# Optimization experiments

Hardware: AMD Instinct MI355X
Metric: run time of the kernel (lower is better)

The kernel has to match this reference:

```python
import jax, jax.numpy as jnp
import numpy as np

DIM = 512
HEADS = 8
WIN = 64
HIDDEN = 2048
EPS = 1e-5


def layernorm(x, g, b):
    mu = jnp.mean(x, axis=-1, keepdims=True)
    var = jnp.var(x, axis=-1, keepdims=True)
    return (x - mu) * jax.lax.rsqrt(var + EPS) * g + b


def setup_inputs() -> dict:
    key = jax.random.key(0)
    ks = jax.random.split(key, 10)
    s = lambda fan_in: 1.0 / np.sqrt(fan_in)
    return {
        "x": jax.random.normal(ks[0], (8, 4096, DIM), dtype=jnp.float32),
        "ln1_g": jnp.ones((DIM,), jnp.float32),
        "ln1_b": jnp.zeros((DIM,), jnp.float32),
        "qkv_w": jax.random.normal(ks[1], (DIM, 3 * DIM), jnp.float32) * s(DIM),
        "qkv_b": jnp.zeros((3 * DIM,), jnp.float32),
        "proj_w": jax.random.normal(ks[2], (DIM, DIM), jnp.float32) * s(DIM),
        "proj_b": jnp.zeros((DIM,), jnp.float32),
        "ln2_g": jnp.ones((DIM,), jnp.float32),
        "ln2_b": jnp.zeros((DIM,), jnp.float32),
        "fc1_w": jax.random.normal(ks[3], (DIM, HIDDEN), jnp.float32) * s(DIM),
        "fc1_b": jnp.zeros((HIDDEN,), jnp.float32),
        "fc2_w": jax.random.normal(ks[4], (HIDDEN, DIM), jnp.float32) * s(HIDDEN),
        "fc2_b": jnp.zeros((DIM,), jnp.float32),
    }


def reference(x, ln1_g, ln1_b, qkv_w, qkv_b, proj_w, proj_b, ln2_g, ln2_b,
              fc1_w, fc1_b, fc2_w, fc2_b):
    B, N, C = x.shape
    hd = C // HEADS
    scale = hd ** -0.5

    # --- W-MSA (shift_size forced to 0, attn_mask None) ---
    h = layernorm(x, ln1_g, ln1_b)
    hw = h.reshape(B * (N // WIN), WIN, C)
    qkv = hw @ qkv_w + qkv_b
    qkv = qkv.reshape(-1, WIN, 3, HEADS, hd)
    q = qkv[:, :, 0] * scale
    k = qkv[:, :, 1]
    v = qkv[:, :, 2]
    attn = jnp.einsum('bqhd,bkhd->bhqk', q, k)
    attn = jax.nn.softmax(attn, axis=-1)
    o = jnp.einsum('bhqk,bkhd->bqhd', attn, v).reshape(-1, WIN, C)
    o = o @ proj_w + proj_b
    x = x + o.reshape(B, N, C)

    # --- MLP (GELU exact, dropout=0) ---
    h2 = layernorm(x, ln2_g, ln2_b)
    h2 = jax.nn.gelu(h2 @ fc1_w + fc1_b, approximate=False)
    x = x + (h2 @ fc2_w + fc2_b)
    return x
```

## Files before the change

kernel.cpp:

```cpp
#include <hip/hip_runtime.h>
#include <hip/hip_bf16.h>
#include <cstdint>

typedef unsigned short U16;
typedef float f32x4 __attribute__((ext_vector_type(4)));
typedef __bf16 bf16x8 __attribute__((ext_vector_type(8)));

#define DEVINL __device__ __forceinline__

DEVINL U16 f2bf(float f) {
    unsigned u = __float_as_uint(f);
    return (U16)((u + 0x7FFFu + ((u >> 16) & 1u)) >> 16);
}
DEVINL float bf2f(U16 s) { return __uint_as_float(((unsigned)s) << 16); }

DEVINL void gld16(const void* g, void* l) {
    __builtin_amdgcn_global_load_lds(
        (const __attribute__((address_space(1))) void*)g,
        (__attribute__((address_space(3))) void*)l, 16, 0, 0);
}

#define MFMA_BF16 __builtin_amdgcn_mfma_f32_16x16x32_bf16

__global__ __launch_bounds__(256) void tcast_kernel(const float* __restrict__ w,
                                                    U16* __restrict__ wt, int K, int N) {
    __shared__ float tile[32][33];
    int n0 = blockIdx.x * 32, k0 = blockIdx.y * 32;
    int tx = threadIdx.x, ty = threadIdx.y;
#pragma unroll
    for (int i = 0; i < 32; i += 8) tile[ty + i][tx] = w[(size_t)(k0 + ty + i) * N + (n0 + tx)];
    __syncthreads();
#pragma unroll
    for (int i = 0; i < 32; i += 8) wt[(size_t)(n0 + ty + i) * K + (k0 + tx)] = f2bf(tile[tx][ty + i]);
}

__global__ __launch_bounds__(256) void ln_kernel(const float* __restrict__ x,
                                                 const float* __restrict__ g,
                                                 const float* __restrict__ b,
                                                 U16* __restrict__ out) {
    int lane = threadIdx.x & 63;
    size_t row = (size_t)blockIdx.x * 4 + (threadIdx.x >> 6);
    const float4* xr = (const float4*)(x + row * 512);
    float4 v0 = xr[lane], v1 = xr[lane + 64];
    float s = (v0.x + v0.y) + (v0.z + v0.w) + (v1.x + v1.y) + (v1.z + v1.w);
    float sq = (v0.x * v0.x + v0.y * v0.y + v0.z * v0.z + v0.w * v0.w) +
               (v1.x * v1.x + v1.y * v1.y + v1.z * v1.z + v1.w * v1.w);
#pragma unroll
    for (int m = 1; m < 64; m <<= 1) { s += __shfl_xor(s, m); sq += __shfl_xor(sq, m); }
    float mu = s * (1.f / 512.f);
    float var = sq * (1.f / 512.f) - mu * mu;
    float rs = rsqrtf(var + 1e-5f);
    const float4* g4 = (const float4*)g;
    const float4* b4 = (const float4*)b;
    float4 gv = g4[lane], bv = b4[lane];
    ushort4 o;
    o.x = f2bf((v0.x - mu) * rs * gv.x + bv.x);
    o.y = f2bf((v0.y - mu) * rs * gv.y + bv.y);
    o.z = f2bf((v0.z - mu) * rs * gv.z + bv.z);
    o.w = f2bf((v0.w - mu) * rs * gv.w + bv.w);
    ((ushort4*)(out + row * 512))[lane] = o;
    gv = g4[lane + 64]; bv = b4[lane + 64];
    o.x = f2bf((v1.x - mu) * rs * gv.x + bv.x);
    o.y = f2bf((v1.y - mu) * rs * gv.y + bv.y);
    o.z = f2bf((v1.z - mu) * rs * gv.z + bv.z);
    o.w = f2bf((v1.w - mu) * rs * gv.w + bv.w);
    ((ushort4*)(out + row * 512))[lane + 64] = o;
}

template <int EPI, int K>
__global__ __launch_bounds__(256, 4) void gemm_rt(const U16* __restrict__ A,
                                                  const U16* __restrict__ Bt,
                                                  const float* __restrict__ bias,
                                                  const float* __restrict__ resid,
                                                  U16* __restrict__ outb,
                                                  float* __restrict__ outf,
                                                  int M, int N, int gridN) {
    __shared__ __align__(16) U16 smem[24576];

    const int tid = threadIdx.x;
    const int lane = tid & 63, wv = tid >> 6;
    const int lo = lane & 15, hi = lane >> 4;
    const int wm = wv >> 1, wn = wv & 1;

    const int nwg = gridDim.x, bid = blockIdx.x;
    const int swzb = (bid & 7) * (nwg >> 3) + (bid >> 3);
    const int bn = swzb % gridN, bm = swzb / gridN;

    const int sr = tid >> 2;
    const int lc = (tid & 3) ^ ((sr >> 1) & 3);
    const U16* gA0 = A + (size_t)(bm * 128 + sr) * K + lc * 8;
    const U16* gA1 = gA0 + (size_t)64 * K;
    const U16* gB0 = Bt + (size_t)(bn * 128 + sr) * K + lc * 8;
    const U16* gB1 = gB0 + (size_t)64 * K;

#define STAGE(t2)                                                     \
    do {                                                              \
        U16* _l = smem + ((t2) % 3) * 8192 + tid * 8;                 \
        gld16(gA0 + (t2) * 32, _l);                                   \
        gld16(gA1 + (t2) * 32, _l + 2048);                            \
        gld16(gB0 + (t2) * 32, _l + 4096);                            \
        gld16(gB1 + (t2) * 32, _l + 6144);                            \
    } while (0)

    const int ck = (hi ^ ((lo >> 1) & 3)) << 3;
    const int aoff = (wm * 64 + lo) * 32 + ck;
    const int boff = 4096 + (wn * 64 + lo) * 32 + ck;

    f32x4 acc[4][4] = {};

    constexpr int NT = K >> 5;
    static_assert(NT >= 16 && (NT % 16) == 0, "K must be a multiple of 512");

    STAGE(0);
    STAGE(1);

#define ITER(t)                                                                 \
    do {                                                                        \
        if ((t) + 1 < NT) {                                                     \
            asm volatile("s_waitcnt vmcnt(4)" ::: "memory");                    \
        } else {                                                                \
            asm volatile("s_waitcnt vmcnt(0)" ::: "memory");                    \
        }                                                                       \
        __builtin_amdgcn_s_barrier();                                           \
        if ((t) + 2 < NT) STAGE((t) + 2);                                       \
        {                                                                       \
            const int _cb = ((t) % 3) * 8192;                                   \
            const U16* _Ab = smem + _cb + aoff;                                 \
            const U16* _Bb = smem + _cb + boff;                                 \
            bf16x8 af[4], bg[4];                                                \
            _Pragma("unroll") for (int i = 0; i < 4; ++i)                       \
                af[i] = *(const bf16x8*)(_Ab + i * 512);                        \
            _Pragma("unroll") for (int j = 0; j < 4; ++j)                       \
                bg[j] = *(const bf16x8*)(_Bb + j * 512);                        \
            __builtin_amdgcn_s_setprio(1);                                      \
            _Pragma("unroll") for (int i = 0; i < 4; ++i)                       \
                _Pragma("unroll") for (int j = 0; j < 4; ++j)                   \
                    acc[i][j] = MFMA_BF16(af[i], bg[j], acc[i][j], 0, 0, 0);    \
            __builtin_amdgcn_s_setprio(0);                                      \
        }                                                                       \
    } while (0)

#pragma unroll
    for (int t0 = 0; t0 < NT; t0 += 16) {
#pragma unroll
        for (int tt = 0; tt < 16; ++tt) ITER(t0 + tt);
    }

    const int row0 = bm * 128 + wm * 64 + hi * 4;
    const int col0 = bn * 128 + wn * 64 + lo;
    float bc[4];
#pragma unroll
    for (int j = 0; j < 4; ++j) bc[j] = bias[col0 + j * 16];

    if (EPI == 1) {
#pragma unroll
        for (int i = 0; i < 4; ++i)
#pragma unroll
            for (int r = 0; r < 4; ++r) {
                const size_t rowb = (size_t)(row0 + i * 16 + r) * N;
#pragma unroll
                for (int j = 0; j < 4; ++j) {
                    const size_t idx = rowb + col0 + j * 16;
                    outf[idx] = acc[i][j][r] + bc[j] + resid[idx];
                }
            }
    } else {
#pragma unroll
        for (int i = 0; i < 4; ++i)
#pragma unroll
            for (int j = 0; j < 4; ++j)
#pragma unroll
                for (int r = 0; r < 4; ++r) {
                    float v = acc[i][j][r] + bc[j];
                    if (EPI == 2) {
                        float u = v * (0.7978845608028654f + 0.0356774081f * v * v);
                        v = v / (1.f + __expf(-2.f * u));
                    }
                    outb[(size_t)(row0 + i * 16 + r) * N + col0 + j * 16] = f2bf(v);
                }
    }
#undef ITER
#undef STAGE
}

__global__ __launch_bounds__(256) void attn_kernel(const U16* __restrict__ qkv,
                                                   U16* __restrict__ o) {
    const int blk = blockIdx.x;
    const int w = blk >> 3, h = blk & 7;
    const int tid = threadIdx.x;
    const int lane = tid & 63, wv = tid >> 6;
    const int lo = lane & 15, hi = lane >> 4;

    __shared__ __align__(16) U16 Qs[64][72];
    __shared__ __align__(16) U16 Ks[64][72];
    __shared__ __align__(16) U16 Vt[64][72];
    __shared__ __align__(16) U16 Ps[4][16][72];

    {
        const int r = tid >> 2;
        const int c0 = (tid & 3) << 4;
        const U16* p = qkv + (size_t)(w * 64 + r) * 1536 + h * 64 + c0;
        *(bf16x8*)&Ks[r][c0] = *(const bf16x8*)(p + 512);
        *(bf16x8*)&Ks[r][c0 + 8] = *(const bf16x8*)(p + 520);
        const U16* pv = p + 1024;
#pragma unroll
        for (int i = 0; i < 16; i++) Vt[c0 + i][r] = pv[i];
#pragma unroll
        for (int i = 0; i < 16; i++) Qs[r][c0 + i] = f2bf(bf2f(p[i]) * 0.125f);
    }
    __syncthreads();

    const int rb = wv * 16;
    f32x4 s[4] = {};
#pragma unroll
    for (int dc = 0; dc < 64; dc += 32) {
        bf16x8 a = *(const bf16x8*)&Qs[rb + lo][dc + hi * 8];
#pragma unroll
        for (int jb = 0; jb < 4; jb++) {
            bf16x8 bfr = *(const bf16x8*)&Ks[jb * 16 + lo][dc + hi * 8];
            s[jb] = MFMA_BF16(a, bfr, s[jb], 0, 0, 0);
        }
    }
#pragma unroll
    for (int r = 0; r < 4; r++) {
        float m = fmaxf(fmaxf(s[0][r], s[1][r]), fmaxf(s[2][r], s[3][r]));
#pragma unroll
        for (int msk = 1; msk < 16; msk <<= 1) m = fmaxf(m, __shfl_xor(m, msk));
        float e[4], sum = 0.f;
#pragma unroll
        for (int jb = 0; jb < 4; jb++) { e[jb] = __expf(s[jb][r] - m); sum += e[jb]; }
#pragma unroll
        for (int msk = 1; msk < 16; msk <<= 1) sum += __shfl_xor(sum, msk);
        float inv = 1.f / sum;
#pragma unroll
        for (int jb = 0; jb < 4; jb++) Ps[wv][hi * 4 + r][jb * 16 + lo] = f2bf(e[jb] * inv);
    }
    __syncthreads();

    f32x4 oa[4] = {};
#pragma unroll
    for (int jc = 0; jc < 64; jc += 32) {
        bf16x8 a = *(const bf16x8*)&Ps[wv][lo][jc + hi * 8];
#pragma unroll
        for (int db = 0; db < 4; db++) {
            bf16x8 bfr = *(const bf16x8*)&Vt[db * 16 + lo][jc + hi * 8];
            oa[db] = MFMA_BF16(a, bfr, oa[db], 0, 0, 0);
        }
    }
#pragma unroll
    for (int db = 0; db < 4; db++)
#pragma unroll
        for (int r = 0; r < 4; r++)
            o[(size_t)(w * 64 + rb + hi * 4 + r) * 512 + h * 64 + db * 16 + lo] = f2bf(oa[db][r]);
}

extern "C" void kernel_launch(void* const* d_in, const int* in_sizes, int n_in,
                              void* d_out, int out_size, void* d_ws, size_t ws_size,
                              hipStream_t stream) {
    const float* x = (const float*)d_in[0];
    const float* ln1_g = (const float*)d_in[1];
    const float* ln1_b = (const float*)d_in[2];
    const float* qkv_w = (const float*)d_in[3];
    const float* qkv_b = (const float*)d_in[4];
    const float* proj_w = (const float*)d_in[5];
    const float* proj_b = (const float*)d_in[6];
    const float* ln2_g = (const float*)d_in[7];
    const float* ln2_b = (const float*)d_in[8];
    const float* fc1_w = (const float*)d_in[9];
    const float* fc1_b = (const float*)d_in[10];
    const float* fc2_w = (const float*)d_in[11];
    const float* fc2_b = (const float*)d_in[12];
    float* out = (float*)d_out;

    char* ws = (char*)d_ws;
    U16* hbuf = (U16*)ws;
    U16* big = (U16*)(ws + 33554432);
    U16* wt_qkv = (U16*)(ws + 33554432 + 134217728);
    U16* wt_proj = wt_qkv + 1536 * 512;
    U16* wt_fc1 = wt_proj + 512 * 512;
    U16* wt_fc2 = wt_fc1 + 2048 * 512;

    dim3 tb(32, 8);
    tcast_kernel<<<dim3(1536 / 32, 512 / 32), tb, 0, stream>>>(qkv_w, wt_qkv, 512, 1536);
    tcast_kernel<<<dim3(512 / 32, 512 / 32), tb, 0, stream>>>(proj_w, wt_proj, 512, 512);
    tcast_kernel<<<dim3(2048 / 32, 512 / 32), tb, 0, stream>>>(fc1_w, wt_fc1, 512, 2048);
    tcast_kernel<<<dim3(512 / 32, 2048 / 32), tb, 0, stream>>>(fc2_w, wt_fc2, 2048, 512);

    ln_kernel<<<8192, 256, 0, stream>>>(x, ln1_g, ln1_b, hbuf);
    gemm_rt<0, 512><<<3072, 256, 0, stream>>>(hbuf, wt_qkv, qkv_b, nullptr, big, nullptr, 32768, 1536, 12);
    attn_kernel<<<4096, 256, 0, stream>>>(big, hbuf);
    gemm_rt<1, 512><<<1024, 256, 0, stream>>>(hbuf, wt_proj, proj_b, x, nullptr, out, 32768, 512, 4);
    ln_kernel<<<8192, 256, 0, stream>>>(out, ln2_g, ln2_b, hbuf);
    gemm_rt<2, 512><<<4096, 256, 0, stream>>>(hbuf, wt_fc1, fc1_b, nullptr, big, nullptr, 32768, 2048, 16);
    gemm_rt<1, 2048><<<1024, 256, 0, stream>>>(big, wt_fc2, fc2_b, out, nullptr, out, 32768, 512, 4);
}
```

Before: 380.5 us.

## Enlarge GEMM tiles to 256x256 with 8 waves and a four-stage LDS ring

The GEMM block tile grows from 128x128 to 256x256, using 512 threads. Each wave now computes a 128x64 sub-tile, and the LDS ring grows to four stages (128KB). A and B tile loads are issued as separate prefetches interleaved between two MFMA half-phases. The goal is more operand reuse per byte loaded and better overlap of global-to-LDS traffic with compute. In exchange, each CU holds only one block, the accumulator register load is larger, and the proj and fc2 GEMMs launch only 256 blocks, which risks tail and latency-hiding problems.

```diff
diff --git a/kernel.cpp b/kernel.cpp
--- a/kernel.cpp
+++ b/kernel.cpp
@@ -68,19 +68,19 @@
 }
 
 template <int EPI, int K>
-__global__ __launch_bounds__(256, 4) void gemm_rt(const U16* __restrict__ A,
+__global__ __launch_bounds__(512, 1) void gemm_rt(const U16* __restrict__ A,
                                                   const U16* __restrict__ Bt,
                                                   const float* __restrict__ bias,
                                                   const float* __restrict__ resid,
                                                   U16* __restrict__ outb,
                                                   float* __restrict__ outf,
                                                   int M, int N, int gridN) {
-    __shared__ __align__(16) U16 smem[24576];
+    __shared__ __align__(16) U16 smem[65536];
 
     const int tid = threadIdx.x;
     const int lane = tid & 63, wv = tid >> 6;
     const int lo = lane & 15, hi = lane >> 4;
-    const int wm = wv >> 1, wn = wv & 1;
+    const int wm = wv >> 2, wn = wv & 3;
 
     const int nwg = gridDim.x, bid = blockIdx.x;
     const int swzb = (bid & 7) * (nwg >> 3) + (bid >> 3);
@@ -88,31 +88,35 @@
 
     const int sr = tid >> 2;
     const int lc = (tid & 3) ^ ((sr >> 1) & 3);
-    const U16* gA0 = A + (size_t)(bm * 128 + sr) * K + lc * 8;
-    const U16* gA1 = gA0 + (size_t)64 * K;
-    const U16* gB0 = Bt + (size_t)(bn * 128 + sr) * K + lc * 8;
-    const U16* gB1 = gB0 + (size_t)64 * K;
-
-#define STAGE(t2)                                                     \
+    const U16* gA0 = A + (size_t)(bm * 256 + sr) * K + lc * 8;
+    const U16* gA1 = gA0 + (size_t)128 * K;
+    const U16* gB0 = Bt + (size_t)(bn * 256 + sr) * K + lc * 8;
+    const U16* gB1 = gB0 + (size_t)128 * K;
+
+#define STAGE_A(t2)                                                   \
     do {                                                              \
-        U16* _l = smem + ((t2) % 3) * 8192 + tid * 8;                 \
+        U16* _l = smem + ((t2) & 3) * 16384 + tid * 8;                \
         gld16(gA0 + (t2) * 32, _l);                                   \
-        gld16(gA1 + (t2) * 32, _l + 2048);                            \
-        gld16(gB0 + (t2) * 32, _l + 4096);                            \
-        gld16(gB1 + (t2) * 32, _l + 6144);                            \
+        gld16(gA1 + (t2) * 32, _l + 4096);                            \
     } while (0)
+#define STAGE_B(t2)                                                   \
+    do {                                                              \
+        U16* _l = smem + ((t2) & 3) * 16384 + 8192 + tid * 8;         \
+        gld16(gB0 + (t2) * 32, _l);                                   \
+        gld16(gB1 + (t2) * 32, _l + 4096);                            \
+    } while (0)
 
     const int ck = (hi ^ ((lo >> 1) & 3)) << 3;
-    const int aoff = (wm * 64 + lo) * 32 + ck;
-    const int boff = 4096 + (wn * 64 + lo) * 32 + ck;
-
-    f32x4 acc[4][4] = {};
+    const int aoff = (wm * 128 + lo) * 32 + ck;
+    const int boff = 8192 + (wn * 64 + lo) * 32 + ck;
+
+    f32x4 acc[8][4] = {};
 
     constexpr int NT = K >> 5;
     static_assert(NT >= 16 && (NT % 16) == 0, "K must be a multiple of 512");
 
-    STAGE(0);
-    STAGE(1);
+    STAGE_A(0); STAGE_B(0);
+    STAGE_A(1); STAGE_B(1);
 
 #define ITER(t)                                                                 \
     do {                                                                        \
@@ -122,11 +126,12 @@
             asm volatile("s_waitcnt vmcnt(0)" ::: "memory");                    \
         }                                                                       \
         __builtin_amdgcn_s_barrier();                                           \
-        if ((t) + 2 < NT) STAGE((t) + 2);                                       \
         {                                                                       \
-            const int _cb = ((t) % 3) * 8192;                                   \
+            const int _cb = ((t) & 3) * 16384;                                  \
             const U16* _Ab = smem + _cb + aoff;                                 \
             const U16* _Bb = smem + _cb + boff;                                 \
+               \
+            if ((t) + 2 < NT) STAGE_A((t) + 2);                                 \
             bf16x8 af[4], bg[4];                                                \
             _Pragma("unroll") for (int i = 0; i < 4; ++i)                       \
                 af[i] = *(const bf16x8*)(_Ab + i * 512);                        \
@@ -137,6 +142,16 @@
                 _Pragma("unroll") for (int j = 0; j < 4; ++j)                   \
                     acc[i][j] = MFMA_BF16(af[i], bg[j], acc[i][j], 0, 0, 0);    \
             __builtin_amdgcn_s_setprio(0);                                      \
+                              \
+            if ((t) + 2 < NT) STAGE_B((t) + 2);                                 \
+            bf16x8 af2[4];                                                      \
+            _Pragma("unroll") for (int i = 0; i < 4; ++i)                       \
+                af2[i] = *(const bf16x8*)(_Ab + (i + 4) * 512);                 \
+            __builtin_amdgcn_s_setprio(1);                                      \
+            _Pragma("unroll") for (int i = 0; i < 4; ++i)                       \
+                _Pragma("unroll") for (int j = 0; j < 4; ++j)                   \
+                    acc[4 + i][j] = MFMA_BF16(af2[i], bg[j], acc[4 + i][j], 0, 0, 0); \
+            __builtin_amdgcn_s_setprio(0);                                      \
         }                                                                       \
     } while (0)
 
@@ -146,15 +161,15 @@
         for (int tt = 0; tt < 16; ++tt) ITER(t0 + tt);
     }
 
-    const int row0 = bm * 128 + wm * 64 + hi * 4;
-    const int col0 = bn * 128 + wn * 64 + lo;
+    const int row0 = bm * 256 + wm * 128 + hi * 4;
+    const int col0 = bn * 256 + wn * 64 + lo;
     float bc[4];
 #pragma unroll
     for (int j = 0; j < 4; ++j) bc[j] = bias[col0 + j * 16];
 
     if (EPI == 1) {
 #pragma unroll
-        for (int i = 0; i < 4; ++i)
+        for (int i = 0; i < 8; ++i)
 #pragma unroll
             for (int r = 0; r < 4; ++r) {
                 const size_t rowb = (size_t)(row0 + i * 16 + r) * N;
@@ -166,7 +181,7 @@
             }
     } else {
 #pragma unroll
-        for (int i = 0; i < 4; ++i)
+        for (int i = 0; i < 8; ++i)
 #pragma unroll
             for (int j = 0; j < 4; ++j)
 #pragma unroll
@@ -180,7 +195,8 @@
                 }
     }
 #undef ITER
-#undef STAGE
+#undef STAGE_A
+#undef STAGE_B
 }
 
 __global__ __launch_bounds__(256) void attn_kernel(const U16* __restrict__ qkv,
@@ -287,10 +303,10 @@
     tcast_kernel<<<dim3(512 / 32, 2048 / 32), tb, 0, stream>>>(fc2_w, wt_fc2, 2048, 512);
 
     ln_kernel<<<8192, 256, 0, stream>>>(x, ln1_g, ln1_b, hbuf);
-    gemm_rt<0, 512><<<3072, 256, 0, stream>>>(hbuf, wt_qkv, qkv_b, nullptr, big, nullptr, 32768, 1536, 12);
+    gemm_rt<0, 512><<<768, 512, 0, stream>>>(hbuf, wt_qkv, qkv_b, nullptr, big, nullptr, 32768, 1536, 6);
     attn_kernel<<<4096, 256, 0, stream>>>(big, hbuf);
-    gemm_rt<1, 512><<<1024, 256, 0, stream>>>(hbuf, wt_proj, proj_b, x, nullptr, out, 32768, 512, 4);
+    gemm_rt<1, 512><<<256, 512, 0, stream>>>(hbuf, wt_proj, proj_b, x, nullptr, out, 32768, 512, 2);
     ln_kernel<<<8192, 256, 0, stream>>>(out, ln2_g, ln2_b, hbuf);
-    gemm_rt<2, 512><<<4096, 256, 0, stream>>>(hbuf, wt_fc1, fc1_b, nullptr, big, nullptr, 32768, 2048, 16);
-    gemm_rt<1, 2048><<<1024, 256, 0, stream>>>(big, wt_fc2, fc2_b, out, nullptr, out, 32768, 512, 4);
-}
+    gemm_rt<2, 512><<<1024, 512, 0, stream>>>(hbuf, wt_fc1, fc1_b, nullptr, big, nullptr, 32768, 2048, 8);
+    gemm_rt<1, 2048><<<256, 512, 0, stream>>>(big, wt_fc2, fc2_b, out, nullptr, out, 32768, 512, 2);
+}
```

Result: faster. 363.2 us (-4.5%).
